# Kernel tuning notes

Hardware: AMD Instinct MI355X
Metric: run time of the kernel (lower is better)

The kernel has to match this reference:

```python
import jax, jax.numpy as jnp
import numpy as np

B, L, IN = 4, 2048, 64
D, N, K, NL, NC = 256, 16, 32, 2, 2


def _ln(x, g, b):
    m = x.mean(-1, keepdims=True)
    v = ((x - m) ** 2).mean(-1, keepdims=True)
    return (x - m) * jax.lax.rsqrt(v + 1e-5) * g + b


def _dwconv(x, w, b):
    # depthwise conv1d, kernel 3, padding 1; x: [B,L,D], w: [D,3]
    xp = jnp.pad(x, ((0, 0), (1, 1), (0, 0)))
    return xp[:, :-2] * w[:, 0] + xp[:, 1:-1] * w[:, 1] + xp[:, 2:] * w[:, 2] + b


def _ssm(x, loglam, wd, bd, wb, wc, wo, bo):
    # x: [B,L,D]
    lam = jax.nn.softplus(loglam)                      # [D,N]
    delta = jax.nn.softplus(x @ wd + bd)[..., None]    # [B,L,D,1]
    Bt = (x @ wb)[:, :, None, :]                       # [B,L,1,N]
    Ct = (x @ wc)[:, :, None, :]                       # [B,L,1,N]
    A_d = jnp.exp(-delta * lam)                        # [B,L,D,N]
    B_d = delta * Bt                                   # [B,L,D,N]
    A_l = jnp.moveaxis(A_d, 1, 0)                      # [L,B,D,N]
    B_l = jnp.moveaxis(B_d, 1, 0)

    def step(h, ab):
        a, b = ab
        h = a * h + b
        return h, h

    h0 = jnp.zeros((x.shape[0], D, N), x.dtype)
    _, hs = jax.lax.scan(step, h0, (A_l, B_l))         # [L,B,D,N]
    ys = hs * jnp.moveaxis(Ct, 1, 0)                   # [L,B,D,N]
    out = jnp.moveaxis(ys, 0, 1).reshape(x.shape[0], x.shape[1], D * N)
    return out @ wo + bo


def _temporal_block(x, lg, lb, cw, cb, loglam, wd, bd, wb, wc, wo, bo, gw, gb, pw, pb):
    res = x
    xn = _ln(x, lg, lb)
    xc = _dwconv(xn, cw, cb)
    xs = _ssm(xc, loglam, wd, bd, wb, wc, wo, bo)
    g = jax.nn.sigmoid(xn @ gw + gb)
    return (xs * g) @ pw + pb + res


def _spectral(x, fr, fi):
    X = jnp.fft.rfft(x, axis=1)                        # [B,F,D] complex64
    mag = jnp.abs(X).mean(axis=(0, 2))                 # [F]
    k = min(K, X.shape[1])
    _, idx = jax.lax.top_k(mag, k)
    filt = (fr[:, :k] + 1j * fi[:, :k]).T              # [k,D]
    Xk = X[:, idx, :] * filt[None]
    Xo = jnp.zeros(X.shape, X.dtype).at[:, idx, :].set(Xk)
    return jnp.fft.irfft(Xo, n=x.shape[1], axis=1)


def setup_inputs() -> dict:
    key = jax.random.key(0)
    ks = jax.random.split(key, 32)
    rn = lambda i, shape, s=0.02: jax.random.normal(ks[i], shape, jnp.float32) * s
    inp = {
        "x": jax.random.normal(ks[0], (B, L, IN), jnp.float32),
        "w_in": rn(1, (IN, D), 0.1), "b_in": jnp.zeros((D,), jnp.float32),
        "ln_g": jnp.ones((NL, D), jnp.float32), "ln_b": jnp.zeros((NL, D), jnp.float32),
        "conv_w": rn(2, (NL, D, 3), 0.3), "conv_b": jnp.zeros((NL, D), jnp.float32),
        "loglam": jax.random.uniform(ks[3], (NL, D, N), jnp.float32),
        "wd": rn(4, (NL, D, D), 0.05), "bd": jnp.zeros((NL, D), jnp.float32),
        "wb": rn(5, (NL, D, N), 0.05), "wc": rn(6, (NL, D, N), 0.05),
        "wo": rn(7, (NL, D * N, D), 0.01), "bo": jnp.zeros((NL, D), jnp.float32),
        "gate_w": rn(8, (NL, D, D), 0.05), "gate_b": jnp.zeros((NL, D), jnp.float32),
        "proj_w": rn(9, (NL, D, D), 0.05), "proj_b": jnp.zeros((NL, D), jnp.float32),
        "fr": rn(10, (D, K)), "fi": rn(11, (D, K)),
        "alpha": jnp.full((D,), 0.5, jnp.float32), "beta": jnp.full((D,), 0.5, jnp.float32),
        "g_out": jnp.ones((D,), jnp.float32), "b_out": jnp.zeros((D,), jnp.float32),
        "hw1": rn(12, (D, D // 2), 0.05), "hb1": jnp.zeros((D // 2,), jnp.float32),
        "hw2": rn(13, (D // 2, NC), 0.05), "hb2": jnp.zeros((NC,), jnp.float32),
    }
    return inp


def reference(x, w_in, b_in, ln_g, ln_b, conv_w, conv_b, loglam, wd, bd, wb, wc, wo, bo,
              gate_w, gate_b, proj_w, proj_b, fr, fi, alpha, beta, g_out, b_out,
              hw1, hb1, hw2, hb2):
    h = x @ w_in + b_in                                # [B,L,D]
    xt = h
    for i in range(NL):
        xt = _temporal_block(xt, ln_g[i], ln_b[i], conv_w[i], conv_b[i], loglam[i],
                             wd[i], bd[i], wb[i], wc[i], wo[i], bo[i],
                             gate_w[i], gate_b[i], proj_w[i], proj_b[i])
    xs = _spectral(h, fr, fi)
    z = alpha * xt + beta * xs
    z = _ln(z, g_out, b_out)
    zl = z[:, -1, :]                                   # [B,D]
    hid = jax.nn.silu(zl @ hw1 + hb1)                  # dropout is identity in eval
    return hid @ hw2 + hb2                             # [B,NC]
```

## Files before the change

kernel.cpp:

```cpp
#include <hip/hip_runtime.h>
#include <hip/hip_bf16.h>
#include <math.h>

#define BB   4
#define LL   2048
#define INF_ 64
#define DD   256
#define NN   16
#define KK   32
#define BLn  (BB*LL)
#define FCNT 1025
#define FSTR 1056
#define SKM  8192
#define SKN  256
#define PSZ  ((size_t)SKM * SKN)
#define IX(x) ((x) + ((x) >> 6))

typedef short short8 __attribute__((ext_vector_type(8)));
typedef float f32x4  __attribute__((ext_vector_type(4)));

__device__ __forceinline__ float softplusf(float x) {
    return x > 20.f ? x : log1pf(__expf(x));
}
__device__ __forceinline__ float sigmoidf_(float x) {
    return 1.f / (1.f + __expf(-x));
}

__global__ void twiddle_kernel(float* tab) {
    int i = blockIdx.x * 256 + threadIdx.x;
    if (i < 2048) {
        double ang = 2.0 * 3.14159265358979323846 * (double)i / 2048.0;
        tab[i]        = (float)cos(ang);
        tab[2048 + i] = (float)sin(ang);
    }
}

__global__ void tcast_kernel(const float* __restrict__ W, __hip_bfloat16* __restrict__ Wt,
                             int K, int N) {
    __shared__ float t[32][33];
    const int k0 = blockIdx.y * 32, n0 = blockIdx.x * 32;
    const int tx = threadIdx.x & 31, ty = threadIdx.x >> 5;
    for (int r = ty; r < 32; r += 8) t[r][tx] = W[(size_t)(k0 + r) * N + n0 + tx];
    __syncthreads();
    for (int r = ty; r < 32; r += 8)
        Wt[(size_t)(n0 + r) * K + k0 + tx] = __float2bfloat16(t[tx][r]);
}

__global__ void pack16_kernel(const float* __restrict__ wb, const float* __restrict__ wc,
                              __hip_bfloat16* __restrict__ cat) {
    const int j = blockIdx.x;
    const int k = threadIdx.x;
    const float* src = (j < 16) ? wb : wc;
    const int jj = j & 15;
    cat[(size_t)(256 + j) * 256 + k] = __float2bfloat16(src[k * 16 + jj]);
}

__global__ void htrans_kernel(const float* __restrict__ h, float* __restrict__ ht) {
    __shared__ float t[32][33];
    const int b = blockIdx.z;
    const int l0 = blockIdx.x * 32, d0 = blockIdx.y * 32;
    const int tx = threadIdx.x & 31, ty = threadIdx.x >> 5;
    for (int r = ty; r < 32; r += 8)
        t[r][tx] = h[((size_t)b * LL + l0 + r) * DD + d0 + tx];
    __syncthreads();
    for (int r = ty; r < 32; r += 8)
        ht[((size_t)b * DD + d0 + r) * LL + l0 + tx] = t[tx][r];
}

__global__ void gemm64(const float* __restrict__ A, const float* __restrict__ W,
                       const float* __restrict__ bias, float* __restrict__ C,
                       int M, int N, int K) {
    __shared__ float As[16][68];
    __shared__ float Ws[16][64];
    const int tid = threadIdx.x;
    const int tx = tid & 15, ty = tid >> 4;
    const int row0 = blockIdx.y * 64, col0 = blockIdx.x * 64;
    float acc[4][4] = {};
    for (int k0 = 0; k0 < K; k0 += 16) {
#pragma unroll
        for (int e = 0; e < 4; ++e) {
            int p = e * 256 + tid;
            As[p & 15][p >> 4] = A[(size_t)(row0 + (p >> 4)) * K + k0 + (p & 15)];
        }
#pragma unroll
        for (int e = 0; e < 4; ++e) {
            int p = e * 256 + tid;
            Ws[p >> 6][p & 63] = W[(size_t)(k0 + (p >> 6)) * N + col0 + (p & 63)];
        }
        __syncthreads();
#pragma unroll
        for (int kk = 0; kk < 16; ++kk) {
            float4 a4 = *(const float4*)&As[kk][ty * 4];
            float4 w4 = *(const float4*)&Ws[kk][tx * 4];
            float av[4] = {a4.x, a4.y, a4.z, a4.w};
            float wv[4] = {w4.x, w4.y, w4.z, w4.w};
#pragma unroll
            for (int i = 0; i < 4; ++i)
#pragma unroll
                for (int j = 0; j < 4; ++j)
                    acc[i][j] = fmaf(av[i], wv[j], acc[i][j]);
        }
        __syncthreads();
    }
#pragma unroll
    for (int i = 0; i < 4; ++i) {
        int r = row0 + ty * 4 + i;
#pragma unroll
        for (int j = 0; j < 4; ++j) {
            int c = col0 + tx * 4 + j;
            C[(size_t)r * N + c] = acc[i][j] + bias[c];
        }
    }
}

template<int MODE>
__global__ __launch_bounds__(256)
void gemm_core(const short* __restrict__ A, const short* __restrict__ Bw,
               const float* __restrict__ bias, const float* __restrict__ x1,
               const float* __restrict__ x2, float* __restrict__ o0,
               float* __restrict__ o1, float* __restrict__ o2,
               __hip_bfloat16* __restrict__ ob) {
    __shared__ alignas(16) short As[2][64][40];
    __shared__ alignas(16) short Bs[2][64][40];
    const int tid = threadIdx.x;
    const int w = tid >> 6, lane = tid & 63;
    const int hi = lane >> 4, lo = lane & 15;
    const int row0 = blockIdx.y * 64, col0 = blockIdx.x * 64;
    f32x4 acc[4];
    f32x4 zz = {0.f, 0.f, 0.f, 0.f};
#pragma unroll
    for (int n = 0; n < 4; ++n) acc[n] = zz;
    const int sr = tid >> 2, sc = (tid & 3) * 8;
    short8 pa = *(const short8*)&A[(size_t)(row0 + sr) * 256 + sc];
    short8 pb = *(const short8*)&Bw[(size_t)(col0 + sr) * 256 + sc];
    *(short8*)&As[0][sr][sc] = pa;
    *(short8*)&Bs[0][sr][sc] = pb;
    pa = *(const short8*)&A[(size_t)(row0 + sr) * 256 + 32 + sc];
    pb = *(const short8*)&Bw[(size_t)(col0 + sr) * 256 + 32 + sc];
    __syncthreads();
    int cur = 0;
    for (int it = 0; it < 8; ++it) {
        if (it + 1 < 8) {
            *(short8*)&As[cur ^ 1][sr][sc] = pa;
            *(short8*)&Bs[cur ^ 1][sr][sc] = pb;
        }
        if (it + 2 < 8) {
            const int k0 = (it + 2) << 5;
            pa = *(const short8*)&A[(size_t)(row0 + sr) * 256 + k0 + sc];
            pb = *(const short8*)&Bw[(size_t)(col0 + sr) * 256 + k0 + sc];
        }
        short8 af = *(const short8*)&As[cur][w * 16 + lo][hi * 8];
        short8 bfr[4];
#pragma unroll
        for (int n = 0; n < 4; ++n)
            bfr[n] = *(const short8*)&Bs[cur][n * 16 + lo][hi * 8];
#pragma unroll
        for (int n = 0; n < 4; ++n)
            acc[n] = __builtin_amdgcn_mfma_f32_16x16x32_bf16(af, bfr[n], acc[n], 0, 0, 0);
        __syncthreads();
        cur ^= 1;
    }
#pragma unroll
    for (int n = 0; n < 4; ++n) {
#pragma unroll
        for (int r = 0; r < 4; ++r) {
            const int row = row0 + w * 16 + hi * 4 + r;
            const int col = col0 + n * 16 + lo;
            float v = acc[n][r];
            if constexpr (MODE == 0) {
                if (col < 256)      o0[(size_t)row * 256 + col] = softplusf(v + bias[col]);
                else if (col < 272) o1[(size_t)row * 16 + col - 256] = v;
                else if (col < 288) o2[(size_t)row * 16 + col - 272] = v;
            } else if constexpr (MODE == 1) {
                float g = sigmoidf_(v + bias[col]);
                float s = x1[(size_t)row * 256 + col] + x1[PSZ + (size_t)row * 256 + col] + x2[col];
                ob[(size_t)row * 256 + col] = __float2bfloat16(g * s);
            } else {
                o0[(size_t)row * 256 + col] = v + bias[col] + x1[(size_t)row * 256 + col];
            }
        }
    }
}

__global__ __launch_bounds__(256)
void gemm_sk_kernel(const __hip_bfloat16* __restrict__ Abf, const __hip_bfloat16* __restrict__ Wt,
                    float* __restrict__ P) {
    __shared__ alignas(16) short As[2][128][40];
    __shared__ alignas(16) short Bs[2][64][40];
    const int tid = threadIdx.x;
    const int f = blockIdx.x;
    const int xcd = f & 7, slot = f >> 3;
    const int col = slot & 3;
    const int rk = xcd + (slot >> 2) * 8;
    const int row = rk & 63, kb = rk >> 6;
    const int row0 = row * 128, col0 = col * 64;
    const size_t kbase = (size_t)kb * 2048;
    const int w = tid >> 6, lane = tid & 63;
    const int hi = lane >> 4, lo = lane & 15;
    const short* A = (const short*)Abf;
    const short* B = (const short*)Wt;
    f32x4 acc[2][4];
    f32x4 zz = {0.f, 0.f, 0.f, 0.f};
#pragma unroll
    for (int m = 0; m < 2; ++m)
#pragma unroll
        for (int n = 0; n < 4; ++n) acc[m][n] = zz;
    const int ra0 = tid >> 2,          ca0 = (tid & 3) * 8;
    const int ra1 = (256 + tid) >> 2,  ca1 = ((256 + tid) & 3) * 8;
    short8 pa0 = *(const short8*)&A[(size_t)(row0 + ra0) * 4096 + kbase + ca0];
    short8 pa1 = *(const short8*)&A[(size_t)(row0 + ra1) * 4096 + kbase + ca1];
    short8 pb  = *(const short8*)&B[(size_t)(col0 + ra0) * 4096 + kbase + ca0];
    *(short8*)&As[0][ra0][ca0] = pa0;
    *(short8*)&As[0][ra1][ca1] = pa1;
    *(short8*)&Bs[0][ra0][ca0] = pb;
    pa0 = *(const short8*)&A[(size_t)(row0 + ra0) * 4096 + kbase + 32 + ca0];
    pa1 = *(const short8*)&A[(size_t)(row0 + ra1) * 4096 + kbase + 32 + ca1];
    pb  = *(const short8*)&B[(size_t)(col0 + ra0) * 4096 + kbase + 32 + ca0];
    __syncthreads();
    int cur = 0;
    for (int it = 0; it < 64; ++it) {
        if (it + 1 < 64) {
            *(short8*)&As[cur ^ 1][ra0][ca0] = pa0;
            *(short8*)&As[cur ^ 1][ra1][ca1] = pa1;
            *(short8*)&Bs[cur ^ 1][ra0][ca0] = pb;
        }
        if (it + 2 < 64) {
            const size_t k0 = kbase + ((it + 2) << 5);
            pa0 = *(const short8*)&A[(size_t)(row0 + ra0) * 4096 + k0 + ca0];
            pa1 = *(const short8*)&A[(size_t)(row0 + ra1) * 4096 + k0 + ca1];
            pb  = *(const short8*)&B[(size_t)(col0 + ra0) * 4096 + k0 + ca0];
        }
        short8 af[2], bfr[4];
#pragma unroll
        for (int m = 0; m < 2; ++m)
            af[m] = *(const short8*)&As[cur][w * 32 + m * 16 + lo][hi * 8];
#pragma unroll
        for (int n = 0; n < 4; ++n)
            bfr[n] = *(const short8*)&Bs[cur][n * 16 + lo][hi * 8];
#pragma unroll
        for (int m = 0; m < 2; ++m)
#pragma unroll
            for (int n = 0; n < 4; ++n)
                acc[m][n] = __builtin_amdgcn_mfma_f32_16x16x32_bf16(af[m], bfr[n], acc[m][n], 0, 0, 0);
        __syncthreads();
        cur ^= 1;
    }
    float* Pk = P + (size_t)kb * PSZ;
#pragma unroll
    for (int m = 0; m < 2; ++m)
#pragma unroll
        for (int n = 0; n < 4; ++n)
#pragma unroll
            for (int r = 0; r < 4; ++r) {
                int rr = row0 + w * 32 + m * 16 + hi * 4 + r;
                int cc = col0 + n * 16 + lo;
                Pk[(size_t)rr * SKN + cc] = acc[m][n][r];
            }
}

__global__ void ln_kernel(const float* __restrict__ X, const float* __restrict__ g,
                          const float* __restrict__ b, __hip_bfloat16* __restrict__ Ybf) {
    __shared__ float red[256];
    const int row = blockIdx.x, tid = threadIdx.x;
    const size_t base = (size_t)row * DD;
    float v = X[base + tid];
    red[tid] = v; __syncthreads();
    for (int s = 128; s > 0; s >>= 1) { if (tid < s) red[tid] += red[tid + s]; __syncthreads(); }
    float m = red[0] * (1.f / DD);
    __syncthreads();
    float c = v - m;
    red[tid] = c * c; __syncthreads();
    for (int s = 128; s > 0; s >>= 1) { if (tid < s) red[tid] += red[tid + s]; __syncthreads(); }
    float var = red[0] * (1.f / DD);
    Ybf[base + tid] = __float2bfloat16(c * rsqrtf(var + 1e-5f) * g[tid] + b[tid]);
}

__global__ void conv_kernel(const __hip_bfloat16* __restrict__ Xn, const float* __restrict__ cw,
                            const float* __restrict__ cb, __hip_bfloat16* __restrict__ Xcbf) {
    const size_t i = (size_t)blockIdx.x * 256 + threadIdx.x;
    const int d = (int)(i & 255);
    const int l = (int)((i >> 8) & (LL - 1));
    float w0 = cw[d * 3 + 0], w1 = cw[d * 3 + 1], w2 = cw[d * 3 + 2];
    float xm = (l > 0)      ? __bfloat162float(Xn[i - DD]) : 0.f;
    float x0 = __bfloat162float(Xn[i]);
    float xp = (l < LL - 1) ? __bfloat162float(Xn[i + DD]) : 0.f;
    Xcbf[i] = __float2bfloat16(fmaf(w0, xm, fmaf(w1, x0, fmaf(w2, xp, cb[d]))));
}

template<int PHASE>
__global__ void ssm_chunk_kernel(const float* __restrict__ delta, const float* __restrict__ Bt,
                                 const float* __restrict__ Ct, const float* __restrict__ loglam,
                                 const float* __restrict__ hstart,
                                 float* __restrict__ sA, float* __restrict__ sB,
                                 __hip_bfloat16* __restrict__ ys) {
    __shared__ float dl[128][16];
    __shared__ float btl[128][16];
    __shared__ float ctl[128][16];
    const int dblk = blockIdx.x, c = blockIdx.y, b = blockIdx.z;
    const int tid = threadIdx.x;
    const size_t lbase = (size_t)b * LL + c * 128;
    for (int i = tid; i < 2048; i += 256) {
        int l = i >> 4, q = i & 15;
        dl[l][q]  = delta[(lbase + l) * DD + dblk * 16 + q];
        btl[l][q] = Bt[(lbase + l) * NN + q];
        if (PHASE == 1) ctl[l][q] = Ct[(lbase + l) * NN + q];
    }
    __syncthreads();
    const int dloc = tid >> 4, n = tid & 15;
    const float lam = softplusf(loglam[(dblk * 16 + dloc) * NN + n]);
    float hv = 0.f, ap = 1.f;
    if (PHASE == 1) hv = hstart[((size_t)(b * 16 + c)) * 4096 + dblk * 256 + tid];
    for (int l = 0; l < 128; ++l) {
        float dv = dl[l][dloc];
        float a = __expf(-dv * lam);
        hv = fmaf(a, hv, dv * btl[l][n]);
        if (PHASE == 0) ap *= a;
        else ys[(lbase + l) * (DD * NN) + dblk * 256 + tid] = __float2bfloat16(hv * ctl[l][n]);
    }
    if (PHASE == 0) {
        size_t oi = ((size_t)(b * 16 + c)) * 4096 + dblk * 256 + tid;
        sA[oi] = ap; sB[oi] = hv;
    }
}

__global__ void ssm_comb_kernel(const float* __restrict__ sA, const float* __restrict__ sB,
                                float* __restrict__ hstart, float* __restrict__ hfin) {
    const int id = blockIdx.x * 256 + threadIdx.x;
    const int b = id >> 12, col = id & 4095;
    float h = 0.f;
#pragma unroll
    for (int c = 0; c < 16; ++c) {
        size_t oi = ((size_t)(b * 16 + c)) * 4096 + col;
        hstart[oi] = h;
        h = fmaf(sA[oi], h, sB[oi]);
    }
    if (hfin) hfin[(size_t)b * 4096 + col] = h;
}

__global__ void last_ssm_part_kernel(const float* __restrict__ hfin, const float* __restrict__ Ct,
                                     const float* __restrict__ wo, float* __restrict__ part) {
    __shared__ float hC[4][128];
    const int c = blockIdx.x, tid = threadIdx.x;
    const int p0 = c * 128;
#pragma unroll
    for (int e = 0; e < 2; ++e) {
        int i = e * 256 + tid;
        int b = i >> 7, p = i & 127;
        hC[b][p] = hfin[b * 4096 + p0 + p] *
                   Ct[((size_t)b * LL + (LL - 1)) * NN + (p & 15)];
    }
    __syncthreads();
    float a0 = 0.f, a1 = 0.f, a2 = 0.f, a3 = 0.f;
    for (int p = 0; p < 128; ++p) {
        float wv = wo[(size_t)(p0 + p) * DD + tid];
        a0 = fmaf(hC[0][p], wv, a0);
        a1 = fmaf(hC[1][p], wv, a1);
        a2 = fmaf(hC[2][p], wv, a2);
        a3 = fmaf(hC[3][p], wv, a3);
    }
    part[(0 * 32 + c) * DD + tid] = a0;
    part[(1 * 32 + c) * DD + tid] = a1;
    part[(2 * 32 + c) * DD + tid] = a2;
    part[(3 * 32 + c) * DD + tid] = a3;
}

__global__ void last_ssm_red_kernel(const float* __restrict__ part, const float* __restrict__ bo,
                                    float* __restrict__ outlast) {
    const int b = blockIdx.x, d = threadIdx.x;
    float acc = bo[d];
#pragma unroll
    for (int c = 0; c < 32; ++c) acc += part[(b * 32 + c) * DD + d];
    outlast[b * DD + d] = acc;
}

__global__ void last_proj_kernel(const __hip_bfloat16* __restrict__ xn, const float* __restrict__ outlast,
                                 const float* __restrict__ gw, const float* __restrict__ gb,
                                 const float* __restrict__ pw, const float* __restrict__ pb,
                                 const float* __restrict__ resid, float* __restrict__ xtlast) {
    __shared__ float xrow[256];
    __shared__ float xsg[256];
    const int b = blockIdx.x, d = threadIdx.x;
    const size_t rbase = ((size_t)b * LL + (LL - 1)) * DD;
    xrow[d] = __bfloat162float(xn[rbase + d]);
    __syncthreads();
    float acc = gb[d];
    for (int k = 0; k < 256; ++k) acc = fmaf(xrow[k], gw[(size_t)k * DD + d], acc);
    float g = sigmoidf_(acc);
    xsg[d] = outlast[b * DD + d] * g;
    __syncthreads();
    float acc2 = pb[d];
    for (int k = 0; k < 256; ++k) acc2 = fmaf(xsg[k], pw[(size_t)k * DD + d], acc2);
    xtlast[b * DD + d] = acc2 + resid[rbase + d];
}

__global__ __launch_bounds__(256)
void fft2_kernel(const float* __restrict__ ht, const float* __restrict__ tab,
                 float* __restrict__ Xre, float* __restrict__ Xim) {
    __shared__ float re[2080];
    __shared__ float im[2080];
    __shared__ float c2[2048];
    __shared__ float s2[2048];
    const int tid = threadIdx.x;
    const int pair = blockIdx.x;
    const int b = pair >> 7, d0 = pair & 127;
    for (int p = tid; p < 2048; p += 256) {
        if (p >= 1) {
            int lh = 31 - __clz((unsigned)p);
            int j = p - (1 << lh);
            int t = j << (10 - lh);
            c2[p] = tab[t]; s2[p] = tab[2048 + t];
        }
    }
    const float* ha = ht + ((size_t)b * 256 + d0) * LL;
    const float* hb = ha + (size_t)128 * LL;
    for (int i = tid; i < 2048; i += 256) {
        int r = (int)(__brev((unsigned)i) >> 21);
        re[IX(r)] = ha[i];
        im[IX(r)] = hb[i];
    }
    __syncthreads();
#pragma unroll
    for (int s = 1; s <= 11; ++s) {
        const int half = 1 << (s - 1);
#pragma unroll
        for (int e = 0; e < 4; ++e) {
            int q = e * 256 + tid;
            int j = q & (half - 1);
            int i0 = ((q >> (s - 1)) << s) + j;
            int i1 = i0 + half;
            float wr = c2[half + j], wi = -s2[half + j];
            float xr = re[IX(i1)], xi = im[IX(i1)];
            float tr = xr * wr - xi * wi;
            float ti = xr * wi + xi * wr;
            float ur = re[IX(i0)], ui = im[IX(i0)];
            re[IX(i0)] = ur + tr; im[IX(i0)] = ui + ti;
            re[IX(i1)] = ur - tr; im[IX(i1)] = ui - ti;
        }
        __syncthreads();
    }
    const int seqa = b * 256 + d0;
    float* xra = Xre + (size_t)seqa * FSTR;
    float* xia = Xim + (size_t)seqa * FSTR;
    float* xrb = xra + (size_t)128 * FSTR;
    float* xib = xia + (size_t)128 * FSTR;
    for (int f = tid; f < FCNT; f += 256) {
        int nf = (2048 - f) & 2047;
        float zrf = re[IX(f)], zif = im[IX(f)];
        float zrn = re[IX(nf)], zin = im[IX(nf)];
        xra[f] = 0.5f * (zrf + zrn);
        xia[f] = 0.5f * (zif - zin);
        xrb[f] = 0.5f * (zif + zin);
        xib[f] = 0.5f * (zrn - zrf);
    }
}

__global__ void mag_part_kernel(const float* __restrict__ Xre, const float* __restrict__ Xim,
                                float* __restrict__ part) {
    const int fb = blockIdx.x, sb = blockIdx.y;
    const int tid = threadIdx.x;
    const int f = fb * 256 + tid;
    float s = 0.f;
    if (f < FCNT) {
        for (int q = 0; q < 64; ++q) {
            size_t base = (size_t)(sb * 64 + q) * FSTR + f;
            float re = Xre[base], im = Xim[base];
            s += sqrtf(re * re + im * im);
        }
    }
    part[sb * 1280 + fb * 256 + tid] = s;
}

__global__ void topk_kernel(const float* __restrict__ part, int* __restrict__ sel) {
    __shared__ float vals[1280];
    __shared__ float wv[4];
    __shared__ int wi[4];
    const int tid = threadIdx.x;
    const int lane = tid & 63, wid = tid >> 6;
    for (int i = tid; i < 1280; i += 256) {
        float v = -1e30f;
        if (i < FCNT) {
            v = 0.f;
#pragma unroll
            for (int sb = 0; sb < 16; ++sb) v += part[sb * 1280 + i];
        }
        vals[i] = v;
    }
    __syncthreads();
    for (int k = 0; k < 32; ++k) {
        float bv = -1e30f; int bi = 0x7fffffff;
        for (int i = tid; i < FCNT; i += 256) {
            float v = vals[i];
            if (v > bv) { bv = v; bi = i; }
        }
#pragma unroll
        for (int off = 32; off > 0; off >>= 1) {
            float ov = __shfl_down(bv, off);
            int   oi = __shfl_down(bi, off);
            if (ov > bv || (ov == bv && oi < bi)) { bv = ov; bi = oi; }
        }
        if (lane == 0) { wv[wid] = bv; wi[wid] = bi; }
        __syncthreads();
        if (tid == 0) {
            float fv = wv[0]; int fi = wi[0];
#pragma unroll
            for (int q = 1; q < 4; ++q)
                if (wv[q] > fv || (wv[q] == fv && wi[q] < fi)) { fv = wv[q]; fi = wi[q]; }
            sel[k] = fi;
            vals[fi] = -1e30f;
        }
        __syncthreads();
    }
}

__global__ void xslast_kernel(const float* __restrict__ Xre, const float* __restrict__ Xim,
                              const int* __restrict__ sel, const float* __restrict__ fr,
                              const float* __restrict__ fi, const float* __restrict__ tab,
                              float* __restrict__ xsl) {
    const int b = blockIdx.x, d = threadIdx.x;
    const size_t sbase = (size_t)(b * 256 + d) * FSTR;
    float acc = 0.f;
    for (int j = 0; j < 32; ++j) {
        int f = sel[j];
        float xr = Xre[sbase + f];
        float xi = Xim[sbase + f];
        float frv = fr[d * KK + j], fiv = fi[d * KK + j];
        float xor_ = xr * frv - xi * fiv;
        float xoi  = xr * fiv + xi * frv;
        int kk2 = (f * (LL - 1)) & (LL - 1);
        float c = tab[kk2], s = tab[2048 + kk2];
        float w = (f == 0 || f == 1024) ? 1.f : 2.f;
        acc = fmaf(w, xor_ * c - xoi * s, acc);
    }
    xsl[b * DD + d] = acc * (1.f / LL);
}

__global__ void head_kernel(const float* __restrict__ xtlast, const float* __restrict__ xslast,
                            const float* __restrict__ alpha, const float* __restrict__ beta,
                            const float* __restrict__ gout, const float* __restrict__ bout,
                            const float* __restrict__ hw1, const float* __restrict__ hb1,
                            const float* __restrict__ hw2, const float* __restrict__ hb2,
                            float* __restrict__ out) {
    __shared__ float red[256];
    __shared__ float z[256];
    __shared__ float hid[128];
    const int b = blockIdx.x, tid = threadIdx.x;
    float zv = alpha[tid] * xtlast[b * 256 + tid] + beta[tid] * xslast[b * 256 + tid];
    red[tid] = zv; __syncthreads();
    for (int s = 128; s > 0; s >>= 1) { if (tid < s) red[tid] += red[tid + s]; __syncthreads(); }
    float m = red[0] * (1.f / DD);
    __syncthreads();
    float c = zv - m;
    red[tid] = c * c; __syncthreads();
    for (int s = 128; s > 0; s >>= 1) { if (tid < s) red[tid] += red[tid + s]; __syncthreads(); }
    float var = red[0] * (1.f / DD);
    z[tid] = c * rsqrtf(var + 1e-5f) * gout[tid] + bout[tid];
    __syncthreads();
    if (tid < 128) {
        float a = hb1[tid];
        for (int k = 0; k < 256; ++k) a = fmaf(z[k], hw1[(size_t)k * 128 + tid], a);
        hid[tid] = a * sigmoidf_(a);
    }
    __syncthreads();
    if (tid < 2) {
        float a = hb2[tid];
        for (int k = 0; k < 128; ++k) a = fmaf(hid[k], hw2[(size_t)k * 2 + tid], a);
        out[b * 2 + tid] = a;
    }
}

extern "C" void kernel_launch(void* const* d_in, const int* in_sizes, int n_in,
                              void* d_out, int out_size, void* d_ws, size_t ws_size,
                              hipStream_t stream) {
    const float* x      = (const float*)d_in[0];
    const float* w_in   = (const float*)d_in[1];
    const float* b_in   = (const float*)d_in[2];
    const float* ln_g   = (const float*)d_in[3];
    const float* ln_b   = (const float*)d_in[4];
    const float* conv_w = (const float*)d_in[5];
    const float* conv_b = (const float*)d_in[6];
    const float* loglam = (const float*)d_in[7];
    const float* wd     = (const float*)d_in[8];
    const float* bd     = (const float*)d_in[9];
    const float* wb     = (const float*)d_in[10];
    const float* wc     = (const float*)d_in[11];
    const float* wo     = (const float*)d_in[12];
    const float* bo     = (const float*)d_in[13];
    const float* gw     = (const float*)d_in[14];
    const float* gb     = (const float*)d_in[15];
    const float* pw     = (const float*)d_in[16];
    const float* pb     = (const float*)d_in[17];
    const float* fr     = (const float*)d_in[18];
    const float* fi     = (const float*)d_in[19];
    const float* alpha  = (const float*)d_in[20];
    const float* beta   = (const float*)d_in[21];
    const float* gout   = (const float*)d_in[22];
    const float* bout   = (const float*)d_in[23];
    const float* hw1    = (const float*)d_in[24];
    const float* hb1    = (const float*)d_in[25];
    const float* hw2    = (const float*)d_in[26];
    const float* hb2    = (const float*)d_in[27];

    float* ws = (float*)d_ws;
    size_t o = 0;
    auto alloc = [&](size_t n) { float* p = ws + o; o += (n + 15) & ~(size_t)15; return p; };

    const size_t BLnDD = (size_t)BLn * DD;
    float* h      = alloc(BLnDD);
    float* xt1    = alloc(BLnDD);
    float* xn     = alloc(BLnDD);
    float* ht     = alloc(BLnDD);
    float* delta  = alloc(BLnDD);
    float* Btm    = alloc((size_t)BLn * NN);
    float* Ctm    = alloc((size_t)BLn * NN);
    float* tab    = alloc(4096);
    float* ysf    = alloc(BLnDD * NN / 2);
    float* sA     = alloc((size_t)BB * 16 * 4096);
    float* sB     = alloc((size_t)BB * 16 * 4096);
    float* hst    = alloc((size_t)BB * 16 * 4096);
    float* xnbf_f = alloc(BLnDD / 2);
    float* xcbf_f = alloc(BLnDD / 2);
    float* xsgf   = alloc(BLnDD / 2);
    float* cat0_f = alloc((size_t)320 * 256 / 2);
    float* cat1_f = alloc((size_t)320 * 256 / 2);
    float* gwt_f  = alloc((size_t)DD * DD / 2);
    float* pwt_f  = alloc((size_t)DD * DD / 2);
    float* wot_f  = alloc((size_t)DD * NN * DD / 2);
    float* magp   = alloc(16 * 1280);
    int*   sel    = (int*)alloc(32);
    float* hfin   = alloc((size_t)BB * DD * NN);
    float* lpart  = alloc((size_t)BB * 32 * DD);
    float* outlast= alloc(BB * DD);
    float* xtlast = alloc(BB * DD);
    float* xslast = alloc(BB * DD);

    __hip_bfloat16* ys    = (__hip_bfloat16*)ysf;
    float*          Xre   = ysf;
    float*          Xim   = ysf + (size_t)1024 * FSTR;
    __hip_bfloat16* xn_bf = (__hip_bfloat16*)xnbf_f;
    __hip_bfloat16* xc_bf = (__hip_bfloat16*)xcbf_f;
    __hip_bfloat16* xsg_bf= (__hip_bfloat16*)xsgf;
    __hip_bfloat16* cat0  = (__hip_bfloat16*)cat0_f;
    __hip_bfloat16* cat1  = (__hip_bfloat16*)cat1_f;
    __hip_bfloat16* gwt   = (__hip_bfloat16*)gwt_f;
    __hip_bfloat16* pwt   = (__hip_bfloat16*)pwt_f;
    __hip_bfloat16* wot   = (__hip_bfloat16*)wot_f;
    float*          Pbuf  = xt1;

    const dim3 blk(256);

    twiddle_kernel<<<8, blk, 0, stream>>>(tab);
    tcast_kernel<<<dim3(8, 8),   blk, 0, stream>>>(wd,                   cat0, DD, DD);
    tcast_kernel<<<dim3(8, 8),   blk, 0, stream>>>(wd + (size_t)DD * DD, cat1, DD, DD);
    pack16_kernel<<<32, blk, 0, stream>>>(wb,            wc,            cat0);
    pack16_kernel<<<32, blk, 0, stream>>>(wb + DD * NN,  wc + DD * NN,  cat1);
    tcast_kernel<<<dim3(8, 8),   blk, 0, stream>>>(gw, gwt, DD, DD);
    tcast_kernel<<<dim3(8, 8),   blk, 0, stream>>>(pw, pwt, DD, DD);
    tcast_kernel<<<dim3(8, 128), blk, 0, stream>>>(wo, wot, DD * NN, DD);

    gemm64<<<dim3(DD / 64, BLn / 64), blk, 0, stream>>>(x, w_in, b_in, h, BLn, DD, INF_);
    htrans_kernel<<<dim3(64, 8, BB), blk, 0, stream>>>(h, ht);

    const dim3 qgrid(5, BLn / 64);
    const dim3 ggrid(4, BLn / 64);
    const dim3 sgrid(16, 16, BB);

    ln_kernel<<<BLn, blk, 0, stream>>>(h, ln_g, ln_b, xn_bf);
    conv_kernel<<<(BLn * DD) / 256, blk, 0, stream>>>(xn_bf, conv_w, conv_b, xc_bf);
    gemm_core<0><<<qgrid, blk, 0, stream>>>((const short*)xc_bf, (const short*)cat0,
                                            bd, nullptr, nullptr, delta, Btm, Ctm, nullptr);
    ssm_chunk_kernel<0><<<sgrid, blk, 0, stream>>>(delta, Btm, nullptr, loglam,
                                                   nullptr, sA, sB, nullptr);
    ssm_comb_kernel<<<BB * 4096 / 256, blk, 0, stream>>>(sA, sB, hst, nullptr);
    ssm_chunk_kernel<1><<<sgrid, blk, 0, stream>>>(delta, Btm, Ctm, loglam,
                                                   hst, nullptr, nullptr, ys);
    gemm_sk_kernel<<<512, blk, 0, stream>>>(ys, wot, Pbuf);
    gemm_core<1><<<ggrid, blk, 0, stream>>>((const short*)xn_bf, (const short*)gwt,
                                            gb, Pbuf, bo, nullptr, nullptr, nullptr, xsg_bf);
    gemm_core<2><<<ggrid, blk, 0, stream>>>((const short*)xsg_bf, (const short*)pwt,
                                            pb, h, nullptr, xt1, nullptr, nullptr, nullptr);

    ln_kernel<<<BLn, blk, 0, stream>>>(xt1, ln_g + DD, ln_b + DD, xn_bf);
    conv_kernel<<<(BLn * DD) / 256, blk, 0, stream>>>(xn_bf, conv_w + DD * 3, conv_b + DD, xc_bf);
    gemm_core<0><<<qgrid, blk, 0, stream>>>((const short*)xc_bf, (const short*)cat1,
                                            bd + DD, nullptr, nullptr, delta, Btm, Ctm, nullptr);
    ssm_chunk_kernel<0><<<sgrid, blk, 0, stream>>>(delta, Btm, nullptr, loglam + DD * NN,
                                                   nullptr, sA, sB, nullptr);
    ssm_comb_kernel<<<BB * 4096 / 256, blk, 0, stream>>>(sA, sB, hst, hfin);
    last_ssm_part_kernel<<<32, blk, 0, stream>>>(hfin, Ctm, wo + (size_t)DD * NN * DD, lpart);
    last_ssm_red_kernel<<<BB, blk, 0, stream>>>(lpart, bo + DD, outlast);
    last_proj_kernel<<<BB, blk, 0, stream>>>(xn_bf, outlast, gw + (size_t)DD * DD, gb + DD,
                                             pw + (size_t)DD * DD, pb + DD, xt1, xtlast);

    fft2_kernel<<<512, blk, 0, stream>>>(ht, tab, Xre, Xim);
    mag_part_kernel<<<dim3(5, 16), blk, 0, stream>>>(Xre, Xim, magp);
    topk_kernel<<<1, blk, 0, stream>>>(magp, sel);
    xslast_kernel<<<BB, blk, 0, stream>>>(Xre, Xim, sel, fr, fi, tab, xslast);

    head_kernel<<<BB, blk, 0, stream>>>(xtlast, xslast, alpha, beta, gout, bout,
                                        hw1, hb1, hw2, hb2, (float*)d_out);
}
```

Measured before the change: 315.5 us.

## Fuse prep kernels, LN+conv, input GEMM+transpose; widen split-K k-tile

Merges the twiddle, transpose-cast and pack kernels into one prep launch. The fp32 input GEMM is replaced with a bf16 MFMA kernel that also writes the transposed copy, which removes the separate htrans pass. LayerNorm and depthwise conv become one kernel that uses wave shuffles and shared memory, and the two small last-step kernels are combined. The split-K GEMM moves from a 32-wide to a 64-wide k-step per iteration, trading more LDS for fewer barriers. The input projection is now computed in bf16 instead of fp32, which reduces precision.

```diff
diff --git a/kernel.cpp b/kernel.cpp
--- a/kernel.cpp
+++ b/kernel.cpp
@@ -16,6 +16,7 @@
 #define PSZ  ((size_t)SKM * SKN)
 #define IX(x) ((x) + ((x) >> 6))
 
+typedef short short4v __attribute__((ext_vector_type(4)));
 typedef short short8 __attribute__((ext_vector_type(8)));
 typedef float f32x4  __attribute__((ext_vector_type(4)));
 
@@ -25,91 +26,163 @@
 __device__ __forceinline__ float sigmoidf_(float x) {
     return 1.f / (1.f + __expf(-x));
 }
-
-__global__ void twiddle_kernel(float* tab) {
-    int i = blockIdx.x * 256 + threadIdx.x;
-    if (i < 2048) {
-        double ang = 2.0 * 3.14159265358979323846 * (double)i / 2048.0;
-        tab[i]        = (float)cos(ang);
-        tab[2048 + i] = (float)sin(ang);
-    }
-}
-
-__global__ void tcast_kernel(const float* __restrict__ W, __hip_bfloat16* __restrict__ Wt,
-                             int K, int N) {
+__device__ __forceinline__ short bfs(float v) {
+    __hip_bfloat16 h = __float2bfloat16(v);
+    return *reinterpret_cast<short*>(&h);
+}
+
+__global__ void prep_kernel(const float* __restrict__ wd, const float* __restrict__ gw,
+                            const float* __restrict__ pw, const float* __restrict__ wo,
+                            const float* __restrict__ wb, const float* __restrict__ wc,
+                            const float* __restrict__ w_in, float* __restrict__ tab,
+                            __hip_bfloat16* __restrict__ cat0, __hip_bfloat16* __restrict__ cat1,
+                            __hip_bfloat16* __restrict__ gwt, __hip_bfloat16* __restrict__ pwt,
+                            __hip_bfloat16* __restrict__ wot, __hip_bfloat16* __restrict__ wint) {
     __shared__ float t[32][33];
-    const int k0 = blockIdx.y * 32, n0 = blockIdx.x * 32;
-    const int tx = threadIdx.x & 31, ty = threadIdx.x >> 5;
+    const int tid = threadIdx.x;
+    int blk = blockIdx.x;
+    if (blk < 8) {
+        int i = blk * 256 + tid;
+        if (i < 2048) {
+            double ang = 2.0 * 3.14159265358979323846 * (double)i / 2048.0;
+            tab[i]        = (float)cos(ang);
+            tab[2048 + i] = (float)sin(ang);
+        }
+        return;
+    }
+    blk -= 8;
+    const float* W; __hip_bfloat16* Wt; int K, N, bx, by;
+    if (blk < 64)        { W = wd;                     Wt = cat0; K = 256;  N = 256; bx = blk & 7; by = blk >> 3; }
+    else if (blk < 128)  { int q = blk - 64;  W = wd + 65536; Wt = cat1; K = 256; N = 256; bx = q & 7; by = q >> 3; }
+    else if (blk < 192)  { int q = blk - 128; W = gw;  Wt = gwt;  K = 256;  N = 256; bx = q & 7; by = q >> 3; }
+    else if (blk < 256)  { int q = blk - 192; W = pw;  Wt = pwt;  K = 256;  N = 256; bx = q & 7; by = q >> 3; }
+    else if (blk < 1280) { int q = blk - 256; W = wo;  Wt = wot;  K = 4096; N = 256; bx = q & 7; by = q >> 3; }
+    else if (blk < 1344) {
+        int j = (blk - 1280) & 31;
+        const float* src0 = (blk < 1312) ? wb : wb + DD * NN;
+        const float* src1 = (blk < 1312) ? wc : wc + DD * NN;
+        __hip_bfloat16* cat = (blk < 1312) ? cat0 : cat1;
+        const float* src = (j < 16) ? src0 : src1;
+        cat[(size_t)(256 + j) * 256 + tid] = __float2bfloat16(src[tid * 16 + (j & 15)]);
+        return;
+    } else { int q = blk - 1344; W = w_in; Wt = wint; K = 64; N = 256; bx = q & 7; by = q >> 3; }
+    const int k0 = by * 32, n0 = bx * 32;
+    if (k0 >= K) return;
+    const int tx = tid & 31, ty = tid >> 5;
     for (int r = ty; r < 32; r += 8) t[r][tx] = W[(size_t)(k0 + r) * N + n0 + tx];
     __syncthreads();
     for (int r = ty; r < 32; r += 8)
         Wt[(size_t)(n0 + r) * K + k0 + tx] = __float2bfloat16(t[tx][r]);
 }
 
-__global__ void pack16_kernel(const float* __restrict__ wb, const float* __restrict__ wc,
-                              __hip_bfloat16* __restrict__ cat) {
-    const int j = blockIdx.x;
-    const int k = threadIdx.x;
-    const float* src = (j < 16) ? wb : wc;
-    const int jj = j & 15;
-    cat[(size_t)(256 + j) * 256 + k] = __float2bfloat16(src[k * 16 + jj]);
-}
-
-__global__ void htrans_kernel(const float* __restrict__ h, float* __restrict__ ht) {
-    __shared__ float t[32][33];
-    const int b = blockIdx.z;
-    const int l0 = blockIdx.x * 32, d0 = blockIdx.y * 32;
-    const int tx = threadIdx.x & 31, ty = threadIdx.x >> 5;
-    for (int r = ty; r < 32; r += 8)
-        t[r][tx] = h[((size_t)b * LL + l0 + r) * DD + d0 + tx];
-    __syncthreads();
-    for (int r = ty; r < 32; r += 8)
-        ht[((size_t)b * DD + d0 + r) * LL + l0 + tx] = t[tx][r];
-}
-
-__global__ void gemm64(const float* __restrict__ A, const float* __restrict__ W,
-                       const float* __restrict__ bias, float* __restrict__ C,
-                       int M, int N, int K) {
-    __shared__ float As[16][68];
-    __shared__ float Ws[16][64];
-    const int tid = threadIdx.x;
-    const int tx = tid & 15, ty = tid >> 4;
+__global__ __launch_bounds__(256)
+void gemm_in_kernel(const float* __restrict__ x, const __hip_bfloat16* __restrict__ wint,
+                    const float* __restrict__ b_in, float* __restrict__ h,
+                    float* __restrict__ ht) {
+    __shared__ alignas(16) short As[64][72];
+    __shared__ alignas(16) short Bs[64][72];
+    __shared__ float ts[64][68];
+    const int tid = threadIdx.x;
+    const int w = tid >> 6, lane = tid & 63;
+    const int hi = lane >> 4, lo = lane & 15;
     const int row0 = blockIdx.y * 64, col0 = blockIdx.x * 64;
-    float acc[4][4] = {};
-    for (int k0 = 0; k0 < K; k0 += 16) {
-#pragma unroll
-        for (int e = 0; e < 4; ++e) {
-            int p = e * 256 + tid;
-            As[p & 15][p >> 4] = A[(size_t)(row0 + (p >> 4)) * K + k0 + (p & 15)];
-        }
-#pragma unroll
-        for (int e = 0; e < 4; ++e) {
-            int p = e * 256 + tid;
-            Ws[p >> 6][p & 63] = W[(size_t)(k0 + (p >> 6)) * N + col0 + (p & 63)];
-        }
-        __syncthreads();
-#pragma unroll
-        for (int kk = 0; kk < 16; ++kk) {
-            float4 a4 = *(const float4*)&As[kk][ty * 4];
-            float4 w4 = *(const float4*)&Ws[kk][tx * 4];
-            float av[4] = {a4.x, a4.y, a4.z, a4.w};
-            float wv[4] = {w4.x, w4.y, w4.z, w4.w};
-#pragma unroll
-            for (int i = 0; i < 4; ++i)
-#pragma unroll
-                for (int j = 0; j < 4; ++j)
-                    acc[i][j] = fmaf(av[i], wv[j], acc[i][j]);
-        }
-        __syncthreads();
-    }
-#pragma unroll
-    for (int i = 0; i < 4; ++i) {
-        int r = row0 + ty * 4 + i;
-#pragma unroll
-        for (int j = 0; j < 4; ++j) {
-            int c = col0 + tx * 4 + j;
-            C[(size_t)r * N + c] = acc[i][j] + bias[c];
-        }
+    const short* B = (const short*)wint;
+#pragma unroll
+    for (int e = 0; e < 4; ++e) {
+        int q = e * 256 + tid;
+        int r = q >> 4, c4 = (q & 15) * 4;
+        float4 v = *(const float4*)&x[(size_t)(row0 + r) * 64 + c4];
+        short4v s = {bfs(v.x), bfs(v.y), bfs(v.z), bfs(v.w)};
+        *(short4v*)&As[r][c4] = s;
+    }
+#pragma unroll
+    for (int e = 0; e < 2; ++e) {
+        int q = e * 256 + tid;
+        int r = q >> 3, c8 = (q & 7) * 8;
+        *(short8*)&Bs[r][c8] = *(const short8*)&B[(size_t)(col0 + r) * 64 + c8];
+    }
+    __syncthreads();
+    f32x4 acc[4];
+    f32x4 zz = {0.f, 0.f, 0.f, 0.f};
+#pragma unroll
+    for (int n = 0; n < 4; ++n) acc[n] = zz;
+#pragma unroll
+    for (int s = 0; s < 2; ++s) {
+        short8 af = *(const short8*)&As[w * 16 + lo][s * 32 + hi * 8];
+#pragma unroll
+        for (int n = 0; n < 4; ++n) {
+            short8 bf = *(const short8*)&Bs[n * 16 + lo][s * 32 + hi * 8];
+            acc[n] = __builtin_amdgcn_mfma_f32_16x16x32_bf16(af, bf, acc[n], 0, 0, 0);
+        }
+    }
+#pragma unroll
+    for (int n = 0; n < 4; ++n)
+#pragma unroll
+        for (int r = 0; r < 4; ++r) {
+            const int row = row0 + w * 16 + hi * 4 + r;
+            const int col = col0 + n * 16 + lo;
+            float v = acc[n][r] + b_in[col];
+            h[(size_t)row * 256 + col] = v;
+            ts[n * 16 + lo][w * 16 + hi * 4 + r] = v;
+        }
+    __syncthreads();
+    const int b = row0 >> 11, l0 = row0 & 2047, d0 = col0;
+    const int dr = tid >> 2, seg = tid & 3;
+    float* dst = ht + ((size_t)(b * 256 + d0 + dr)) * LL + l0 + seg * 16;
+#pragma unroll
+    for (int j = 0; j < 4; ++j)
+        *(f32x4*)&dst[j * 4] = *(const f32x4*)&ts[dr][seg * 16 + j * 4];
+}
+
+__global__ __launch_bounds__(256)
+void lnconv_kernel(const float* __restrict__ X, const float* __restrict__ g,
+                   const float* __restrict__ bln, const float* __restrict__ cw,
+                   const float* __restrict__ cb, __hip_bfloat16* __restrict__ xn_bf,
+                   __hip_bfloat16* __restrict__ xc_bf) {
+    __shared__ float xs[34][260];
+    const int tid = threadIdx.x;
+    const int w = tid >> 6, lane = tid & 63;
+    const int blk = blockIdx.x;
+    const int b = (blk * 32) >> 11, L0 = (blk * 32) & 2047;
+    const float4 g4 = *(const float4*)&g[lane * 4];
+    const float4 b4 = *(const float4*)&bln[lane * 4];
+    for (int slot = w; slot < 34; slot += 4) {
+        const int l = L0 - 1 + slot;
+        if (l < 0 || l >= LL) {
+            f32x4 z = {0.f, 0.f, 0.f, 0.f};
+            *(f32x4*)&xs[slot][lane * 4] = z;
+            continue;
+        }
+        float4 v = *(const float4*)&X[((size_t)b * LL + l) * DD + lane * 4];
+        float s = v.x + v.y + v.z + v.w;
+#pragma unroll
+        for (int off = 1; off < 64; off <<= 1) s += __shfl_xor(s, off);
+        float m = s * (1.f / DD);
+        float cx = v.x - m, cy = v.y - m, cz = v.z - m, cw_ = v.w - m;
+        float q = cx * cx + cy * cy + cz * cz + cw_ * cw_;
+#pragma unroll
+        for (int off = 1; off < 64; off <<= 1) q += __shfl_xor(q, off);
+        float inv = rsqrtf(q * (1.f / DD) + 1e-5f);
+        f32x4 y;
+        y[0] = cx * inv * g4.x + b4.x;
+        y[1] = cy * inv * g4.y + b4.y;
+        y[2] = cz * inv * g4.z + b4.z;
+        y[3] = cw_ * inv * g4.w + b4.w;
+        *(f32x4*)&xs[slot][lane * 4] = y;
+        if (slot >= 1 && slot <= 32) {
+            short4v s4 = {bfs(y[0]), bfs(y[1]), bfs(y[2]), bfs(y[3])};
+            *(short4v*)&xn_bf[((size_t)b * LL + l) * DD + lane * 4] = s4;
+        }
+    }
+    __syncthreads();
+    const int d = tid;
+    const float w0 = cw[d * 3 + 0], w1 = cw[d * 3 + 1], w2 = cw[d * 3 + 2], cbd = cb[d];
+    float xm = xs[0][d], x0 = xs[1][d];
+    for (int rw = 0; rw < 32; ++rw) {
+        float xp = xs[rw + 2][d];
+        xc_bf[((size_t)b * LL + L0 + rw) * DD + d] =
+            __float2bfloat16(fmaf(w0, xm, fmaf(w1, x0, fmaf(w2, xp, cbd))));
+        xm = x0; x0 = xp;
     }
 }
 
@@ -172,9 +245,9 @@
                 else if (col < 272) o1[(size_t)row * 16 + col - 256] = v;
                 else if (col < 288) o2[(size_t)row * 16 + col - 272] = v;
             } else if constexpr (MODE == 1) {
-                float g = sigmoidf_(v + bias[col]);
+                float gv = sigmoidf_(v + bias[col]);
                 float s = x1[(size_t)row * 256 + col] + x1[PSZ + (size_t)row * 256 + col] + x2[col];
-                ob[(size_t)row * 256 + col] = __float2bfloat16(g * s);
+                ob[(size_t)row * 256 + col] = __float2bfloat16(gv * s);
             } else {
                 o0[(size_t)row * 256 + col] = v + bias[col] + x1[(size_t)row * 256 + col];
             }
@@ -185,8 +258,8 @@
 __global__ __launch_bounds__(256)
 void gemm_sk_kernel(const __hip_bfloat16* __restrict__ Abf, const __hip_bfloat16* __restrict__ Wt,
                     float* __restrict__ P) {
-    __shared__ alignas(16) short As[2][128][40];
-    __shared__ alignas(16) short Bs[2][64][40];
+    __shared__ alignas(16) short As[2][128][72];
+    __shared__ alignas(16) short Bs[2][64][72];
     const int tid = threadIdx.x;
     const int f = blockIdx.x;
     const int xcd = f & 7, slot = f >> 3;
@@ -205,43 +278,66 @@
     for (int m = 0; m < 2; ++m)
 #pragma unroll
         for (int n = 0; n < 4; ++n) acc[m][n] = zz;
-    const int ra0 = tid >> 2,          ca0 = (tid & 3) * 8;
-    const int ra1 = (256 + tid) >> 2,  ca1 = ((256 + tid) & 3) * 8;
-    short8 pa0 = *(const short8*)&A[(size_t)(row0 + ra0) * 4096 + kbase + ca0];
-    short8 pa1 = *(const short8*)&A[(size_t)(row0 + ra1) * 4096 + kbase + ca1];
-    short8 pb  = *(const short8*)&B[(size_t)(col0 + ra0) * 4096 + kbase + ca0];
-    *(short8*)&As[0][ra0][ca0] = pa0;
-    *(short8*)&As[0][ra1][ca1] = pa1;
-    *(short8*)&Bs[0][ra0][ca0] = pb;
-    pa0 = *(const short8*)&A[(size_t)(row0 + ra0) * 4096 + kbase + 32 + ca0];
-    pa1 = *(const short8*)&A[(size_t)(row0 + ra1) * 4096 + kbase + 32 + ca1];
-    pb  = *(const short8*)&B[(size_t)(col0 + ra0) * 4096 + kbase + 32 + ca0];
+    const int sr = tid >> 3, sc = (tid & 7) * 8;
+    const int sr1 = (256 + tid) >> 3, sc1 = ((256 + tid) & 7) * 8;
+    const int sr2 = (512 + tid) >> 3, sc2 = ((512 + tid) & 7) * 8;
+    const int sr3 = (768 + tid) >> 3, sc3 = ((768 + tid) & 7) * 8;
+    short8 pa0 = *(const short8*)&A[(size_t)(row0 + sr ) * 4096 + kbase + sc ];
+    short8 pa1 = *(const short8*)&A[(size_t)(row0 + sr1) * 4096 + kbase + sc1];
+    short8 pa2 = *(const short8*)&A[(size_t)(row0 + sr2) * 4096 + kbase + sc2];
+    short8 pa3 = *(const short8*)&A[(size_t)(row0 + sr3) * 4096 + kbase + sc3];
+    short8 pb0 = *(const short8*)&B[(size_t)(col0 + sr ) * 4096 + kbase + sc ];
+    short8 pb1 = *(const short8*)&B[(size_t)(col0 + sr1) * 4096 + kbase + sc1];
+    *(short8*)&As[0][sr ][sc ] = pa0;
+    *(short8*)&As[0][sr1][sc1] = pa1;
+    *(short8*)&As[0][sr2][sc2] = pa2;
+    *(short8*)&As[0][sr3][sc3] = pa3;
+    *(short8*)&Bs[0][sr ][sc ] = pb0;
+    *(short8*)&Bs[0][sr1][sc1] = pb1;
+    {
+        const size_t k0 = kbase + 64;
+        pa0 = *(const short8*)&A[(size_t)(row0 + sr ) * 4096 + k0 + sc ];
+        pa1 = *(const short8*)&A[(size_t)(row0 + sr1) * 4096 + k0 + sc1];
+        pa2 = *(const short8*)&A[(size_t)(row0 + sr2) * 4096 + k0 + sc2];
+        pa3 = *(const short8*)&A[(size_t)(row0 + sr3) * 4096 + k0 + sc3];
+        pb0 = *(const short8*)&B[(size_t)(col0 + sr ) * 4096 + k0 + sc ];
+        pb1 = *(const short8*)&B[(size_t)(col0 + sr1) * 4096 + k0 + sc1];
+    }
     __syncthreads();
     int cur = 0;
-    for (int it = 0; it < 64; ++it) {
-        if (it + 1 < 64) {
-            *(short8*)&As[cur ^ 1][ra0][ca0] = pa0;
-            *(short8*)&As[cur ^ 1][ra1][ca1] = pa1;
-            *(short8*)&Bs[cur ^ 1][ra0][ca0] = pb;
-        }
-        if (it + 2 < 64) {
-            const size_t k0 = kbase + ((it + 2) << 5);
-            pa0 = *(const short8*)&A[(size_t)(row0 + ra0) * 4096 + k0 + ca0];
-            pa1 = *(const short8*)&A[(size_t)(row0 + ra1) * 4096 + k0 + ca1];
-            pb  = *(const short8*)&B[(size_t)(col0 + ra0) * 4096 + k0 + ca0];
-        }
-        short8 af[2], bfr[4];
-#pragma unroll
-        for (int m = 0; m < 2; ++m)
-            af[m] = *(const short8*)&As[cur][w * 32 + m * 16 + lo][hi * 8];
-#pragma unroll
-        for (int n = 0; n < 4; ++n)
-            bfr[n] = *(const short8*)&Bs[cur][n * 16 + lo][hi * 8];
-#pragma unroll
-        for (int m = 0; m < 2; ++m)
+    for (int it = 0; it < 32; ++it) {
+        if (it + 1 < 32) {
+            *(short8*)&As[cur ^ 1][sr ][sc ] = pa0;
+            *(short8*)&As[cur ^ 1][sr1][sc1] = pa1;
+            *(short8*)&As[cur ^ 1][sr2][sc2] = pa2;
+            *(short8*)&As[cur ^ 1][sr3][sc3] = pa3;
+            *(short8*)&Bs[cur ^ 1][sr ][sc ] = pb0;
+            *(short8*)&Bs[cur ^ 1][sr1][sc1] = pb1;
+        }
+        if (it + 2 < 32) {
+            const size_t k0 = kbase + (size_t)(it + 2) * 64;
+            pa0 = *(const short8*)&A[(size_t)(row0 + sr ) * 4096 + k0 + sc ];
+            pa1 = *(const short8*)&A[(size_t)(row0 + sr1) * 4096 + k0 + sc1];
+            pa2 = *(const short8*)&A[(size_t)(row0 + sr2) * 4096 + k0 + sc2];
+            pa3 = *(const short8*)&A[(size_t)(row0 + sr3) * 4096 + k0 + sc3];
+            pb0 = *(const short8*)&B[(size_t)(col0 + sr ) * 4096 + k0 + sc ];
+            pb1 = *(const short8*)&B[(size_t)(col0 + sr1) * 4096 + k0 + sc1];
+        }
+#pragma unroll
+        for (int kk = 0; kk < 2; ++kk) {
+            short8 af[2], bfr[4];
+#pragma unroll
+            for (int m = 0; m < 2; ++m)
+                af[m] = *(const short8*)&As[cur][w * 32 + m * 16 + lo][kk * 32 + hi * 8];
 #pragma unroll
             for (int n = 0; n < 4; ++n)
-                acc[m][n] = __builtin_amdgcn_mfma_f32_16x16x32_bf16(af[m], bfr[n], acc[m][n], 0, 0, 0);
+                bfr[n] = *(const short8*)&Bs[cur][n * 16 + lo][kk * 32 + hi * 8];
+#pragma unroll
+            for (int m = 0; m < 2; ++m)
+#pragma unroll
+                for (int n = 0; n < 4; ++n)
+                    acc[m][n] = __builtin_amdgcn_mfma_f32_16x16x32_bf16(af[m], bfr[n], acc[m][n], 0, 0, 0);
+        }
         __syncthreads();
         cur ^= 1;
     }
@@ -256,35 +352,6 @@
                 int cc = col0 + n * 16 + lo;
                 Pk[(size_t)rr * SKN + cc] = acc[m][n][r];
             }
-}
-
-__global__ void ln_kernel(const float* __restrict__ X, const float* __restrict__ g,
-                          const float* __restrict__ b, __hip_bfloat16* __restrict__ Ybf) {
-    __shared__ float red[256];
-    const int row = blockIdx.x, tid = threadIdx.x;
-    const size_t base = (size_t)row * DD;
-    float v = X[base + tid];
-    red[tid] = v; __syncthreads();
-    for (int s = 128; s > 0; s >>= 1) { if (tid < s) red[tid] += red[tid + s]; __syncthreads(); }
-    float m = red[0] * (1.f / DD);
-    __syncthreads();
-    float c = v - m;
-    red[tid] = c * c; __syncthreads();
-    for (int s = 128; s > 0; s >>= 1) { if (tid < s) red[tid] += red[tid + s]; __syncthreads(); }
-    float var = red[0] * (1.f / DD);
-    Ybf[base + tid] = __float2bfloat16(c * rsqrtf(var + 1e-5f) * g[tid] + b[tid]);
-}
-
-__global__ void conv_kernel(const __hip_bfloat16* __restrict__ Xn, const float* __restrict__ cw,
-                            const float* __restrict__ cb, __hip_bfloat16* __restrict__ Xcbf) {
-    const size_t i = (size_t)blockIdx.x * 256 + threadIdx.x;
-    const int d = (int)(i & 255);
-    const int l = (int)((i >> 8) & (LL - 1));
-    float w0 = cw[d * 3 + 0], w1 = cw[d * 3 + 1], w2 = cw[d * 3 + 2];
-    float xm = (l > 0)      ? __bfloat162float(Xn[i - DD]) : 0.f;
-    float x0 = __bfloat162float(Xn[i]);
-    float xp = (l < LL - 1) ? __bfloat162float(Xn[i + DD]) : 0.f;
-    Xcbf[i] = __float2bfloat16(fmaf(w0, xm, fmaf(w1, x0, fmaf(w2, xp, cb[d]))));
 }
 
 template<int PHASE>
@@ -364,29 +431,23 @@
     part[(3 * 32 + c) * DD + tid] = a3;
 }
 
-__global__ void last_ssm_red_kernel(const float* __restrict__ part, const float* __restrict__ bo,
-                                    float* __restrict__ outlast) {
-    const int b = blockIdx.x, d = threadIdx.x;
-    float acc = bo[d];
-#pragma unroll
-    for (int c = 0; c < 32; ++c) acc += part[(b * 32 + c) * DD + d];
-    outlast[b * DD + d] = acc;
-}
-
-__global__ void last_proj_kernel(const __hip_bfloat16* __restrict__ xn, const float* __restrict__ outlast,
-                                 const float* __restrict__ gw, const float* __restrict__ gb,
-                                 const float* __restrict__ pw, const float* __restrict__ pb,
-                                 const float* __restrict__ resid, float* __restrict__ xtlast) {
+__global__ void last_redproj_kernel(const float* __restrict__ part, const float* __restrict__ bo,
+                                    const __hip_bfloat16* __restrict__ xn, const float* __restrict__ gw,
+                                    const float* __restrict__ gb, const float* __restrict__ pw,
+                                    const float* __restrict__ pb, const float* __restrict__ resid,
+                                    float* __restrict__ xtlast) {
     __shared__ float xrow[256];
     __shared__ float xsg[256];
     const int b = blockIdx.x, d = threadIdx.x;
+    float ol = bo[d];
+#pragma unroll
+    for (int c = 0; c < 32; ++c) ol += part[(b * 32 + c) * DD + d];
     const size_t rbase = ((size_t)b * LL + (LL - 1)) * DD;
     xrow[d] = __bfloat162float(xn[rbase + d]);
     __syncthreads();
     float acc = gb[d];
     for (int k = 0; k < 256; ++k) acc = fmaf(xrow[k], gw[(size_t)k * DD + d], acc);
-    float g = sigmoidf_(acc);
-    xsg[d] = outlast[b * DD + d] * g;
+    xsg[d] = ol * sigmoidf_(acc);
     __syncthreads();
     float acc2 = pb[d];
     for (int k = 0; k < 256; ++k) acc2 = fmaf(xsg[k], pw[(size_t)k * DD + d], acc2);
@@ -607,7 +668,7 @@
     const size_t BLnDD = (size_t)BLn * DD;
     float* h      = alloc(BLnDD);
     float* xt1    = alloc(BLnDD);
-    float* xn     = alloc(BLnDD);
+    float* xpad   = alloc(BLnDD);
     float* ht     = alloc(BLnDD);
     float* delta  = alloc(BLnDD);
     float* Btm    = alloc((size_t)BLn * NN);
@@ -625,11 +686,11 @@
     float* gwt_f  = alloc((size_t)DD * DD / 2);
     float* pwt_f  = alloc((size_t)DD * DD / 2);
     float* wot_f  = alloc((size_t)DD * NN * DD / 2);
+    float* wint_f = alloc((size_t)DD * 64 / 2);
     float* magp   = alloc(16 * 1280);
     int*   sel    = (int*)alloc(32);
     float* hfin   = alloc((size_t)BB * DD * NN);
     float* lpart  = alloc((size_t)BB * 32 * DD);
-    float* outlast= alloc(BB * DD);
     float* xtlast = alloc(BB * DD);
     float* xslast = alloc(BB * DD);
 
@@ -644,28 +705,20 @@
     __hip_bfloat16* gwt   = (__hip_bfloat16*)gwt_f;
     __hip_bfloat16* pwt   = (__hip_bfloat16*)pwt_f;
     __hip_bfloat16* wot   = (__hip_bfloat16*)wot_f;
+    __hip_bfloat16* wint  = (__hip_bfloat16*)wint_f;
     float*          Pbuf  = xt1;
 
     const dim3 blk(256);
 
-    twiddle_kernel<<<8, blk, 0, stream>>>(tab);
-    tcast_kernel<<<dim3(8, 8),   blk, 0, stream>>>(wd,                   cat0, DD, DD);
-    tcast_kernel<<<dim3(8, 8),   blk, 0, stream>>>(wd + (size_t)DD * DD, cat1, DD, DD);
-    pack16_kernel<<<32, blk, 0, stream>>>(wb,            wc,            cat0);
-    pack16_kernel<<<32, blk, 0, stream>>>(wb + DD * NN,  wc + DD * NN,  cat1);
-    tcast_kernel<<<dim3(8, 8),   blk, 0, stream>>>(gw, gwt, DD, DD);
-    tcast_kernel<<<dim3(8, 8),   blk, 0, stream>>>(pw, pwt, DD, DD);
-    tcast_kernel<<<dim3(8, 128), blk, 0, stream>>>(wo, wot, DD * NN, DD);
-
-    gemm64<<<dim3(DD / 64, BLn / 64), blk, 0, stream>>>(x, w_in, b_in, h, BLn, DD, INF_);
-    htrans_kernel<<<dim3(64, 8, BB), blk, 0, stream>>>(h, ht);
+    prep_kernel<<<1368, blk, 0, stream>>>(wd, gw, pw, wo, wb, wc, w_in, tab,
+                                          cat0, cat1, gwt, pwt, wot, wint);
+    gemm_in_kernel<<<dim3(4, 128), blk, 0, stream>>>(x, wint, b_in, h, ht);
 
     const dim3 qgrid(5, BLn / 64);
     const dim3 ggrid(4, BLn / 64);
     const dim3 sgrid(16, 16, BB);
 
-    ln_kernel<<<BLn, blk, 0, stream>>>(h, ln_g, ln_b, xn_bf);
-    conv_kernel<<<(BLn * DD) / 256, blk, 0, stream>>>(xn_bf, conv_w, conv_b, xc_bf);
+    lnconv_kernel<<<BLn / 32, blk, 0, stream>>>(h, ln_g, ln_b, conv_w, conv_b, xn_bf, xc_bf);
     gemm_core<0><<<qgrid, blk, 0, stream>>>((const short*)xc_bf, (const short*)cat0,
                                             bd, nullptr, nullptr, delta, Btm, Ctm, nullptr);
     ssm_chunk_kernel<0><<<sgrid, blk, 0, stream>>>(delta, Btm, nullptr, loglam,
@@ -679,17 +732,17 @@
     gemm_core<2><<<ggrid, blk, 0, stream>>>((const short*)xsg_bf, (const short*)pwt,
                                             pb, h, nullptr, xt1, nullptr, nullptr, nullptr);
 
-    ln_kernel<<<BLn, blk, 0, stream>>>(xt1, ln_g + DD, ln_b + DD, xn_bf);
-    conv_kernel<<<(BLn * DD) / 256, blk, 0, stream>>>(xn_bf, conv_w + DD * 3, conv_b + DD, xc_bf);
+    lnconv_kernel<<<BLn / 32, blk, 0, stream>>>(xt1, ln_g + DD, ln_b + DD,
+                                                conv_w + DD * 3, conv_b + DD, xn_bf, xc_bf);
     gemm_core<0><<<qgrid, blk, 0, stream>>>((const short*)xc_bf, (const short*)cat1,
                                             bd + DD, nullptr, nullptr, delta, Btm, Ctm, nullptr);
     ssm_chunk_kernel<0><<<sgrid, blk, 0, stream>>>(delta, Btm, nullptr, loglam + DD * NN,
                                                    nullptr, sA, sB, nullptr);
     ssm_comb_kernel<<<BB * 4096 / 256, blk, 0, stream>>>(sA, sB, hst, hfin);
     last_ssm_part_kernel<<<32, blk, 0, stream>>>(hfin, Ctm, wo + (size_t)DD * NN * DD, lpart);
-    last_ssm_red_kernel<<<BB, blk, 0, stream>>>(lpart, bo + DD, outlast);
-    last_proj_kernel<<<BB, blk, 0, stream>>>(xn_bf, outlast, gw + (size_t)DD * DD, gb + DD,
-                                             pw + (size_t)DD * DD, pb + DD, xt1, xtlast);
+    last_redproj_kernel<<<BB, blk, 0, stream>>>(lpart, bo + DD, xn_bf,
+                                                gw + (size_t)DD * DD, gb + DD,
+                                                pw + (size_t)DD * DD, pb + DD, xt1, xtlast);
 
     fft2_kernel<<<512, blk, 0, stream>>>(ht, tab, Xre, Xim);
     mag_part_kernel<<<dim3(5, 16), blk, 0, stream>>>(Xre, Xim, magp);
```

New measurement: 278.9 us. -11.6%, faster.
